# Kernel tuning notes

Measured on AMD Instinct MI355X. Metric: run time of the kernel, lower is better.

Reference implementation:

```python
import jax, jax.numpy as jnp
import numpy as np

EMBED_DIM = 1024
NUM_HEADS = 16
HEAD_DIM = EMBED_DIM // NUM_HEADS
TGT_LEN = 1024
SRC_LEN = 1024
BSZ = 4


def setup_inputs() -> dict:
    key = jax.random.key(0)
    ks = jax.random.split(key, 7)
    query = jax.random.normal(ks[0], (TGT_LEN, BSZ, EMBED_DIM), dtype=jnp.float32)
    key_t = jax.random.normal(ks[1], (SRC_LEN, BSZ, EMBED_DIM), dtype=jnp.float32)
    # hard 0/1 multiplicative mask applied post-softmax
    hard_attention = jax.random.randint(ks[2], (BSZ, TGT_LEN, SRC_LEN), 0, 2).astype(jnp.float32)
    # xavier_uniform_ on [3E, E]
    limit = float(np.sqrt(6.0 / (3 * EMBED_DIM + EMBED_DIM)))
    in_proj_weight = jax.random.uniform(ks[3], (3 * EMBED_DIM, EMBED_DIM), dtype=jnp.float32,
                                        minval=-limit, maxval=limit)
    in_proj_bias = jnp.zeros((3 * EMBED_DIM,), dtype=jnp.float32)
    limit_o = float(np.sqrt(1.0 / EMBED_DIM))
    out_proj_weight = jax.random.uniform(ks[4], (EMBED_DIM, EMBED_DIM), dtype=jnp.float32,
                                         minval=-limit_o, maxval=limit_o)
    out_proj_bias = jnp.zeros((EMBED_DIM,), dtype=jnp.float32)
    return {
        "query": query,
        "key": key_t,
        "hard_attention": hard_attention,
        "in_proj_weight": in_proj_weight,
        "in_proj_bias": in_proj_bias,
        "out_proj_weight": out_proj_weight,
        "out_proj_bias": out_proj_bias,
    }


def reference(query, key, hard_attention, in_proj_weight, in_proj_bias,
              out_proj_weight, out_proj_bias):
    tgt_len, bsz, embed_dim = query.shape
    src_len = key.shape[0]
    h, hd = NUM_HEADS, embed_dim // NUM_HEADS
    scaling = float(hd) ** -0.5

    # QKV projections (F.linear uses y = x @ W.T + b)
    wq = in_proj_weight[:embed_dim]
    wkv = in_proj_weight[embed_dim:]
    bq = in_proj_bias[:embed_dim]
    bkv = in_proj_bias[embed_dim:]
    q = jnp.einsum('tbe,fe->tbf', query, wq) + bq          # [T,B,E]
    kv = jnp.einsum('sbe,fe->sbf', key, wkv) + bkv          # [S,B,2E]
    k, v = jnp.split(kv, 2, axis=-1)

    q = (q * scaling).reshape(tgt_len, bsz, h, hd).transpose(1, 2, 0, 3)  # [B,H,T,D]
    k = k.reshape(src_len, bsz, h, hd).transpose(1, 2, 0, 3)              # [B,H,S,D]
    v = v.reshape(src_len, bsz, h, hd).transpose(1, 2, 0, 3)              # [B,H,S,D]

    scores = jnp.einsum('bhtd,bhsd->bhts', q, k)            # [B,H,T,S]
    attn = jax.nn.softmax(scores, axis=-1)
    # dropout_p = 0.0 -> identity
    attn = attn * hard_attention[:, None, :, :]             # post-softmax hard mask

    out = jnp.einsum('bhts,bhsd->bhtd', attn, v)            # [B,H,T,D]
    out = out.transpose(2, 0, 1, 3).reshape(tgt_len, bsz, embed_dim)
    out = jnp.einsum('tbe,fe->tbf', out, out_proj_weight) + out_proj_bias

    avg_weights = attn.sum(axis=1) / h                      # [B,T,S]
    return (out, avg_weights)
```

## Files before the change

kernel.cpp:

```cpp
#include <hip/hip_runtime.h>
#include <cstdint>
#include <cstddef>

typedef __bf16 bf16x8 __attribute__((ext_vector_type(8)));
typedef float  f32x4  __attribute__((ext_vector_type(4)));
typedef unsigned short u16x8 __attribute__((ext_vector_type(8)));

__device__ __forceinline__ uint16_t f2bf(float f) {
  uint32_t u = __float_as_uint(f);
  u += 0x7fffu + ((u >> 16) & 1u);
  return (uint16_t)(u >> 16);
}
__device__ __forceinline__ float bf2f(uint16_t u) {
  return __uint_as_float((uint32_t)u << 16);
}
__device__ __forceinline__ uint32_t cvtpk(float lo, float hi) {
  uint32_t r;
  asm("v_cvt_pk_bf16_f32 %0, %1, %2" : "=v"(r) : "v"(lo), "v"(hi));
  return r;
}

__device__ __forceinline__ f32x4 mfma16(bf16x8 a, bf16x8 b, f32x4 c) {
  return __builtin_amdgcn_mfma_f32_16x16x32_bf16(a, b, c, 0, 0, 0);
}

#define GLD_TO_LDS16(gptr, lptr)                                                   \
  __builtin_amdgcn_global_load_lds(                                                \
      (const __attribute__((address_space(1))) void*)(gptr),                       \
      (__attribute__((address_space(3))) void*)(lptr), 16, 0, 0)

__global__ void prep(const float* __restrict__ q, const float* __restrict__ k,
                     const float* __restrict__ w, const float* __restrict__ wo,
                     const float* __restrict__ hard,
                     uint16_t* __restrict__ Xq, uint16_t* __restrict__ Xk,
                     uint16_t* __restrict__ Wb, uint16_t* __restrict__ Wob,
                     uint32_t* __restrict__ bits) {
  const int bid = blockIdx.x;
  if (bid < 12288) {
    int i = bid * 256 + threadIdx.x;
    const float* src;
    uint16_t* dst;
    int off;
    if (i < 1048576)      { src = q;  dst = Xq;  off = i; }
    else if (i < 2097152) { src = k;  dst = Xk;  off = i - 1048576; }
    else if (i < 2883584) { src = w;  dst = Wb;  off = i - 2097152; }
    else                  { src = wo; dst = Wob; off = i - 2883584; }
    float4 v = ((const float4*)src)[off];
    ushort4 o;
    o.x = f2bf(v.x); o.y = f2bf(v.y); o.z = f2bf(v.z); o.w = f2bf(v.w);
    ((ushort4*)dst)[off] = o;
  } else {
    int base = (bid - 12288) * 1024;
#pragma unroll
    for (int c = 0; c < 4; c++) {
      int i = base + c * 256 + threadIdx.x;
      unsigned long long m = __ballot(hard[i] != 0.0f);
      if ((threadIdx.x & 63) == 0) {
        int wd = i >> 5;
        bits[wd]     = (uint32_t)m;
        bits[wd + 1] = (uint32_t)(m >> 32);
      }
    }
  }
}

__global__ __launch_bounds__(256)
void gemm_qkv(const uint16_t* __restrict__ Xq, const uint16_t* __restrict__ Xk,
              const uint16_t* __restrict__ Wb, const float* __restrict__ ipb,
              uint16_t* __restrict__ Qb, uint16_t* __restrict__ Kb,
              uint16_t* __restrict__ Vt) {
  __shared__ __align__(16) char As[128 * 128];
  __shared__ __align__(16) char Bs[128 * 128];
  const int tid  = threadIdx.x;
  const int wave = tid >> 6, lane = tid & 63;
  const int quad = lane >> 4, l16 = lane & 15;
  const int sw = (l16 & 7) << 4;

  const int swz = (blockIdx.x & 7) * 96 + (blockIdx.x >> 3);
  const uint16_t *A, *B;
  const float* bias;
  int bm, bn, mode;
  if (swz < 256) {
    mode = 0; A = Xq; B = Wb; bias = ipb;
    bm = swz >> 3; bn = swz & 7;
  } else {
    mode = 1; A = Xk; B = Wb + (1 << 20); bias = ipb + 1024;
    int t = swz - 256; bm = t >> 4; bn = t & 15;
  }
  const int wm = (wave >> 1) << 6, wn = (wave & 1) << 6;

  const int lrow = lane >> 3;
  const int scol = ((lane & 7) ^ lrow) << 4;
  const char* Ag = (const char*)A + (size_t)(bm * 128) * 2048;
  const char* Bg = (const char*)B + (size_t)(bn * 128) * 2048;

  f32x4 acc[4][4] = {};

  for (int k0 = 0; k0 < 2048; k0 += 128) {
    __syncthreads();
#pragma unroll
    for (int j = 0; j < 4; j++) {
      const int rbase = j * 32 + wave * 8;
      GLD_TO_LDS16(Ag + (size_t)(rbase + lrow) * 2048 + k0 + scol,
                   As + rbase * 128);
      GLD_TO_LDS16(Bg + (size_t)(rbase + lrow) * 2048 + k0 + scol,
                   Bs + rbase * 128);
    }
    __syncthreads();

    bf16x8 af[4][2], bfr[4][2];
#pragma unroll
    for (int i = 0; i < 4; i++) {
      const char* pa = As + (wm + i * 16 + l16) * 128;
      const char* pb = Bs + (wn + i * 16 + l16) * 128;
#pragma unroll
      for (int ks = 0; ks < 2; ks++) {
        af[i][ks]  = *(const bf16x8*)(pa + ((ks * 64 + quad * 16) ^ sw));
        bfr[i][ks] = *(const bf16x8*)(pb + ((ks * 64 + quad * 16) ^ sw));
      }
    }
#pragma unroll
    for (int ks = 0; ks < 2; ks++)
#pragma unroll
      for (int mi = 0; mi < 4; mi++)
#pragma unroll
        for (int ni = 0; ni < 4; ni++)
          acc[mi][ni] = mfma16(af[mi][ks], bfr[ni][ks], acc[mi][ni]);
  }

#pragma unroll
  for (int mi = 0; mi < 4; mi++)
#pragma unroll
    for (int ni = 0; ni < 4; ni++)
#pragma unroll
      for (int r = 0; r < 4; r++) {
        int gi = bm * 128 + wm + mi * 16 + quad * 4 + r;
        int gf = bn * 128 + wn + ni * 16 + l16;
        float c = acc[mi][ni][r] + bias[gf];
        if (mode == 0) {
          c *= 0.125f;
          int t = gi >> 2, b = gi & 3, h = gf >> 6, d = gf & 63;
          Qb[((((size_t)b * 16 + h) * 1024 + t) << 6) + d] = f2bf(c);
        } else {
          int s = gi >> 2, b = gi & 3;
          if (gf < 1024) {
            int h = gf >> 6, d = gf & 63;
            Kb[((((size_t)b * 16 + h) * 1024 + s) << 6) + d] = f2bf(c);
          } else {
            int fv = gf - 1024, h = fv >> 6, d = fv & 63;
            Vt[((((size_t)b * 16 + h) * 64 + d) << 10) + s] = f2bf(c);
          }
        }
      }
}

__global__ __launch_bounds__(256, 2)
void attn_kernel(const uint16_t* __restrict__ qb, const uint16_t* __restrict__ kb,
                 const uint16_t* __restrict__ vtb, const uint32_t* __restrict__ bits,
                 uint16_t* __restrict__ attn_out, float* __restrict__ rlout) {
  __shared__ __align__(16) uint16_t Ks[128 * 64];
  __shared__ __align__(16) uint16_t Vs[64 * 128];
  __shared__ __align__(16) uint16_t Pb[4 * 32 * 128];

  const int bid = blockIdx.x;
  const int xcd = bid & 7, j = bid >> 3;
  const int slab = xcd * 8 + (j >> 3);
  const int b = slab >> 4, h = slab & 15;
  const int t0 = (j & 7) << 7;
  const int tid = threadIdx.x, wave = tid >> 6, lane = tid & 63;
  const int quad = lane >> 4, l16 = lane & 15;
  const int sw = (l16 & 7) << 4;
  const size_t bh = (size_t)b * 16 + h;
  const int tw = t0 + wave * 32;
  const int ta = tw + l16, tb = ta + 16;
  char* PwA = (char*)(Pb + wave * (32 * 128)) + l16 * 256;
  char* PwB = PwA + 16 * 256;

  const uint16_t* qA = qb + ((bh << 10) + ta) * 64;
  bf16x8 aqA0 = *(const bf16x8*)(qA + quad * 8);
  bf16x8 aqA1 = *(const bf16x8*)(qA + 32 + quad * 8);
  bf16x8 aqB0 = *(const bf16x8*)(qA + 1024 + quad * 8);
  bf16x8 aqB1 = *(const bf16x8*)(qA + 1024 + 32 + quad * 8);

  f32x4 accA[4] = {}, accB[4] = {};
  float smA = 0.f, smB = 0.f;

  const int kr = tid >> 3, kc8 = tid & 7;
  const int vr = tid >> 4, vc16 = tid & 15;

  const uint32_t* bA = bits + (((size_t)(b << 10) + ta) << 5);
  const uint32_t* bB = bits + (((size_t)(b << 10) + tb) << 5);

  u16x8 kreg[4], vreg[4];
#pragma unroll
  for (int r = 0; r < 4; r++)
    kreg[r] = *(const u16x8*)(kb + (bh << 16) + (size_t)(r * 256 + tid) * 8);
#pragma unroll
  for (int r = 0; r < 4; r++)
    vreg[r] = *(const u16x8*)(vtb + (((bh << 6) + r * 16 + vr) << 10) + vc16 * 8);
  uint4 uA = *(const uint4*)bA;
  uint4 uB = *(const uint4*)bB;

  for (int sc = 0; sc < 8; sc++) {
    uint32_t wA[4] = {uA.x >> (quad * 4), uA.y >> (quad * 4),
                      uA.z >> (quad * 4), uA.w >> (quad * 4)};
    uint32_t wB[4] = {uB.x >> (quad * 4), uB.y >> (quad * 4),
                      uB.z >> (quad * 4), uB.w >> (quad * 4)};

    __syncthreads();
#pragma unroll
    for (int r = 0; r < 4; r++) {
      const int row = r * 32 + kr;
      *(u16x8*)((char*)Ks + row * 128 + ((kc8 * 16) ^ ((row & 7) << 4))) = kreg[r];
    }
#pragma unroll
    for (int r = 0; r < 4; r++) {
      const int row = r * 16 + vr;
      *(u16x8*)((char*)Vs + row * 256 + ((vc16 * 16) ^ ((row & 7) << 4))) = vreg[r];
    }
    __syncthreads();

    if (sc < 7) {
      const uint16_t* kbase = kb + (bh << 16) + (size_t)(sc + 1) * 8192;
#pragma unroll
      for (int r = 0; r < 4; r++)
        kreg[r] = *(const u16x8*)(kbase + (size_t)(r * 256 + tid) * 8);
#pragma unroll
      for (int r = 0; r < 4; r++)
        vreg[r] = *(const u16x8*)(vtb + (((bh << 6) + r * 16 + vr) << 10) +
                                  (sc + 1) * 128 + vc16 * 8);
      uA = *(const uint4*)(bA + (sc + 1) * 4);
      uB = *(const uint4*)(bB + (sc + 1) * 4);
    }

#pragma unroll
    for (int nn = 0; nn < 8; nn++) {
      const char* kbp = (const char*)Ks + (nn * 16 + l16) * 128;
      bf16x8 bk0 = *(const bf16x8*)(kbp + ((quad * 16) ^ sw));
      bf16x8 bk1 = *(const bf16x8*)(kbp + ((64 + quad * 16) ^ sw));
      f32x4 cA = {}, cB = {};
      cA = mfma16(bk0, aqA0, cA); cA = mfma16(bk1, aqA1, cA);
      cB = mfma16(bk0, aqB0, cB); cB = mfma16(bk1, aqB1, cB);
      const uint32_t mA = wA[nn >> 1] >> ((nn & 1) * 16);
      const uint32_t mB = wB[nn >> 1] >> ((nn & 1) * 16);
      float eA[4], eB[4];
#pragma unroll
      for (int r = 0; r < 4; r++) {
        eA[r] = __expf(cA[r]); smA += eA[r];
        eB[r] = __expf(cB[r]); smB += eB[r];
        eA[r] = ((mA >> r) & 1) ? eA[r] : 0.f;
        eB[r] = ((mB >> r) & 1) ? eB[r] : 0.f;
      }
      const int pc = (nn * 32 + quad * 8) ^ sw;
      *(uint2*)(PwA + pc) = make_uint2(cvtpk(eA[0], eA[1]), cvtpk(eA[2], eA[3]));
      *(uint2*)(PwB + pc) = make_uint2(cvtpk(eB[0], eB[1]), cvtpk(eB[2], eB[3]));
    }

#pragma unroll
    for (int kc = 0; kc < 4; kc++) {
      const int pcb = (kc * 64 + quad * 16) ^ sw;
      bf16x8 apA = *(const bf16x8*)(PwA + pcb);
      bf16x8 apB = *(const bf16x8*)(PwB + pcb);
#pragma unroll
      for (int dt = 0; dt < 4; dt++) {
        bf16x8 bv = *(const bf16x8*)((const char*)Vs + (dt * 16 + l16) * 256 +
                                     ((kc * 64 + quad * 16) ^ sw));
        accA[dt] = mfma16(bv, apA, accA[dt]);
        accB[dt] = mfma16(bv, apB, accB[dt]);
      }
    }
  }

  smA += __shfl_xor(smA, 16); smA += __shfl_xor(smA, 32);
  smB += __shfl_xor(smB, 16); smB += __shfl_xor(smB, 32);
  const float rlA = 1.0f / smA, rlB = 1.0f / smB;
  if (quad == 0) rlout[(bh << 10) + ta] = rlA;
  if (quad == 1) rlout[(bh << 10) + tb] = rlB;

#pragma unroll
  for (int dt = 0; dt < 4; dt++) {
    uint2 oA = make_uint2(cvtpk(accA[dt][0] * rlA, accA[dt][1] * rlA),
                          cvtpk(accA[dt][2] * rlA, accA[dt][3] * rlA));
    *(uint2*)(attn_out + ((size_t)(ta * 4 + b) << 10) + h * 64 + dt * 16 + quad * 4) = oA;
    uint2 oB = make_uint2(cvtpk(accB[dt][0] * rlB, accB[dt][1] * rlB),
                          cvtpk(accB[dt][2] * rlB, accB[dt][3] * rlB));
    *(uint2*)(attn_out + ((size_t)(tb * 4 + b) << 10) + h * 64 + dt * 16 + quad * 4) = oB;
  }
}

__global__ __launch_bounds__(256, 4)
void tail(const uint16_t* __restrict__ qb, const uint16_t* __restrict__ kb,
          const float* __restrict__ rlin, const float* __restrict__ hard,
          const uint16_t* __restrict__ Ao, const uint16_t* __restrict__ Bw,
          const float* __restrict__ opb,
          float* __restrict__ out, float* __restrict__ avgout) {
  __shared__ __align__(16) char smem[16384];
  const int bid = blockIdx.x;
  const int tid = threadIdx.x, wave = tid >> 6, lane = tid & 63;
  const int quad = lane >> 4, l16 = lane & 15;

  if (bid < 512) {
    uint16_t* Ks = (uint16_t*)smem;
    const int xcd = bid & 7, j = bid >> 3;
    const int b  = xcd >> 1;
    const int t0 = ((xcd & 1) * 8 + (j >> 3)) << 6;
    const int s0 = (j & 7) << 7;
    const int sw = (l16 & 7) << 4;
    const int tr = t0 + wave * 16 + l16;
    const int kr = tid >> 3, kc8 = tid & 7;

    float av[8][4] = {};

    u16x8 kreg[4];
    {
      const uint16_t* kb0 = kb + ((((size_t)b * 16) << 10) + s0) * 64;
#pragma unroll
      for (int r = 0; r < 4; r++)
        kreg[r] = *(const u16x8*)(kb0 + (size_t)(r * 256 + tid) * 8);
    }

    for (int hh = 0; hh < 16; hh++) {
      __syncthreads();
#pragma unroll
      for (int r = 0; r < 4; r++) {
        const int row = r * 32 + kr;
        *(u16x8*)((char*)Ks + row * 128 + ((kc8 * 16) ^ ((row & 7) << 4))) = kreg[r];
      }
      __syncthreads();
      if (hh < 15) {
        const uint16_t* kb2 = kb + ((((size_t)b * 16 + hh + 1) << 10) + s0) * 64;
#pragma unroll
        for (int r = 0; r < 4; r++)
          kreg[r] = *(const u16x8*)(kb2 + (size_t)(r * 256 + tid) * 8);
      }

      const size_t bh = (size_t)b * 16 + hh;
      const uint16_t* qrow = qb + ((bh << 10) + tr) * 64;
      bf16x8 aq0 = *(const bf16x8*)(qrow + quad * 8);
      bf16x8 aq1 = *(const bf16x8*)(qrow + 32 + quad * 8);
      const float rl = rlin[(bh << 10) + tr];

#pragma unroll
      for (int n = 0; n < 8; n++) {
        const char* kbp = (const char*)Ks + (n * 16 + l16) * 128;
        bf16x8 bk0 = *(const bf16x8*)(kbp + ((quad * 16) ^ sw));
        bf16x8 bk1 = *(const bf16x8*)(kbp + ((64 + quad * 16) ^ sw));
        f32x4 c = {};
        c = mfma16(bk0, aq0, c);
        c = mfma16(bk1, aq1, c);
#pragma unroll
        for (int r = 0; r < 4; r++) av[n][r] += __expf(c[r]) * rl;
      }
    }

    const float* hrow = hard + (((size_t)(b << 10) + tr) << 10) + s0 + quad * 4;
    float* orow = avgout + ((size_t)(b << 10) + tr) * 1024 + s0 + quad * 4;
#pragma unroll
    for (int n = 0; n < 8; n++) {
      float4 hm = *(const float4*)(hrow + n * 16);
      float4 f;
      f.x = av[n][0] * (hm.x != 0.f ? 0.0625f : 0.f);
      f.y = av[n][1] * (hm.y != 0.f ? 0.0625f : 0.f);
      f.z = av[n][2] * (hm.z != 0.f ? 0.0625f : 0.f);
      f.w = av[n][3] * (hm.w != 0.f ? 0.0625f : 0.f);
      *(float4*)(orow + n * 16) = f;
    }
  } else {
    uint16_t* As = (uint16_t*)smem;
    uint16_t* Bs = (uint16_t*)(smem + 4096);
    const int u = bid - 512;
    const int swz = (u & 7) * 64 + (u >> 3);
    const int bm = swz >> 3, bn = swz & 7;
    const int wm = (wave >> 1) << 5, wn = (wave & 1) << 6;
    const int K = 1024;

    f32x4 acc[2][4] = {};

    for (int k0 = 0; k0 < K; k0 += 32) {
      __syncthreads();
      {
        int c   = wave * 64 + lane;
        int row = c >> 2, kc = c & 3;
        const uint16_t* ga = Ao + (size_t)(bm * 64 + row) * K + k0 + kc * 8;
        GLD_TO_LDS16(ga, As + (size_t)(wave * 64) * 8);
      }
#pragma unroll
      for (int jj = 0; jj < 2; jj++) {
        int c   = wave * 128 + jj * 64 + lane;
        int row = c >> 2, kc = c & 3;
        const uint16_t* gb = Bw + (size_t)(bn * 128 + row) * K + k0 + kc * 8;
        GLD_TO_LDS16(gb, Bs + (size_t)(wave * 128 + jj * 64) * 8);
      }
      __syncthreads();

      bf16x8 af[2], bfr[4];
#pragma unroll
      for (int i = 0; i < 2; i++)
        af[i] = *(const bf16x8*)(As + (wm + i * 16 + l16) * 32 + quad * 8);
#pragma unroll
      for (int i = 0; i < 4; i++)
        bfr[i] = *(const bf16x8*)(Bs + (wn + i * 16 + l16) * 32 + quad * 8);
#pragma unroll
      for (int mi = 0; mi < 2; mi++)
#pragma unroll
        for (int ni = 0; ni < 4; ni++)
          acc[mi][ni] = mfma16(af[mi], bfr[ni], acc[mi][ni]);
    }

#pragma unroll
    for (int mi = 0; mi < 2; mi++)
#pragma unroll
      for (int ni = 0; ni < 4; ni++)
#pragma unroll
        for (int r = 0; r < 4; r++) {
          int gi = bm * 64 + wm + mi * 16 + quad * 4 + r;
          int gf = bn * 128 + wn + ni * 16 + l16;
          out[(size_t)gi * 1024 + gf] = acc[mi][ni][r] + opb[gf];
        }
  }
}

extern "C" void kernel_launch(void* const* d_in, const int* in_sizes, int n_in,
                              void* d_out, int out_size, void* d_ws, size_t ws_size,
                              hipStream_t stream) {
  const float* query = (const float*)d_in[0];
  const float* key   = (const float*)d_in[1];
  const float* hard  = (const float*)d_in[2];
  const float* ipw   = (const float*)d_in[3];
  const float* ipb   = (const float*)d_in[4];
  const float* opw   = (const float*)d_in[5];
  const float* opb   = (const float*)d_in[6];

  char* ws = (char*)d_ws;
  const size_t MB = 1ull << 20;
  uint16_t* Xq  = (uint16_t*)(ws + 0);
  uint16_t* Xk  = (uint16_t*)(ws + 8 * MB);
  uint16_t* Wb  = (uint16_t*)(ws + 16 * MB);
  uint16_t* Wob = (uint16_t*)(ws + 22 * MB);
  uint16_t* Qb  = (uint16_t*)(ws + 24 * MB);
  uint16_t* Kb  = (uint16_t*)(ws + 32 * MB);
  uint16_t* Vt  = (uint16_t*)(ws + 40 * MB);
  uint16_t* AO  = Xq;
  float*    rlws = (float*)(ws + 8 * MB);

  float* out = (float*)d_out;
  float* avg = out + 4194304;
  uint32_t* bits = (uint32_t*)out;

  prep<<<16384, 256, 0, stream>>>(query, key, ipw, opw, hard,
                                  Xq, Xk, Wb, Wob, bits);

  gemm_qkv<<<768, 256, 0, stream>>>(Xq, Xk, Wb, ipb, Qb, Kb, Vt);

  attn_kernel<<<512, 256, 0, stream>>>(Qb, Kb, Vt, bits, AO, rlws);

  tail<<<1024, 256, 0, stream>>>(Qb, Kb, rlws, hard, AO, Wob, opb, out, avg);
}
```

Measured before the change: 227.6 us.

## Deepen out-projection GEMM K-tile with XOR-swizzled LDS and remap avg-weight blocks

The output-projection GEMM branch of the tail kernel now stages 64 bf16 K-elements per iteration instead of 32, using an XOR swizzle on the LDS column to avoid bank conflicts. It issues two MFMA k-steps per barrier pair, which halves the number of syncs and global-to-LDS rounds. Shared memory grows to 24 KB. The avg-weights branch also remaps block indices so each XCD handles contiguous (batch, source-slab) groups, aiming for better L2 locality of K data. The larger LDS footprint may reduce occupancy.

```diff
diff --git a/kernel.cpp b/kernel.cpp
--- a/kernel.cpp
+++ b/kernel.cpp
@@ -294,7 +294,7 @@
           const uint16_t* __restrict__ Ao, const uint16_t* __restrict__ Bw,
           const float* __restrict__ opb,
           float* __restrict__ out, float* __restrict__ avgout) {
-  __shared__ __align__(16) char smem[16384];
+  __shared__ __align__(16) char smem[24576];
   const int bid = blockIdx.x;
   const int tid = threadIdx.x, wave = tid >> 6, lane = tid & 63;
   const int quad = lane >> 4, l16 = lane & 15;
@@ -302,9 +302,10 @@
   if (bid < 512) {
     uint16_t* Ks = (uint16_t*)smem;
     const int xcd = bid & 7, j = bid >> 3;
-    const int b  = xcd >> 1;
-    const int t0 = ((xcd & 1) * 8 + (j >> 3)) << 6;
-    const int s0 = (j & 7) << 7;
+    const int slab = xcd * 4 + (j >> 4);
+    const int b  = slab >> 3;
+    const int s0 = (slab & 7) << 7;
+    const int t0 = (j & 15) << 6;
     const int sw = (l16 & 7) << 4;
     const int tr = t0 + wave * 16 + l16;
     const int kr = tid >> 3, kc8 = tid & 7;
@@ -366,45 +367,58 @@
       *(float4*)(orow + n * 16) = f;
     }
   } else {
-    uint16_t* As = (uint16_t*)smem;
-    uint16_t* Bs = (uint16_t*)(smem + 4096);
+    char* As = smem;
+    char* Bs = smem + 8192;
     const int u = bid - 512;
     const int swz = (u & 7) * 64 + (u >> 3);
     const int bm = swz >> 3, bn = swz & 7;
     const int wm = (wave >> 1) << 5, wn = (wave & 1) << 6;
-    const int K = 1024;
+    const int sw = (l16 & 7) << 4;
+    const int lrow = lane >> 3;
+    const int scol = ((lane & 7) ^ lrow) << 4;
+    const char* Ag = (const char*)Ao + (size_t)(bm * 64) * 2048;
+    const char* Bg = (const char*)Bw + (size_t)(bn * 128) * 2048;
 
     f32x4 acc[2][4] = {};
 
-    for (int k0 = 0; k0 < K; k0 += 32) {
+    for (int k0 = 0; k0 < 2048; k0 += 128) {
       __syncthreads();
-      {
-        int c   = wave * 64 + lane;
-        int row = c >> 2, kc = c & 3;
-        const uint16_t* ga = Ao + (size_t)(bm * 64 + row) * K + k0 + kc * 8;
-        GLD_TO_LDS16(ga, As + (size_t)(wave * 64) * 8);
-      }
 #pragma unroll
       for (int jj = 0; jj < 2; jj++) {
-        int c   = wave * 128 + jj * 64 + lane;
-        int row = c >> 2, kc = c & 3;
-        const uint16_t* gb = Bw + (size_t)(bn * 128 + row) * K + k0 + kc * 8;
-        GLD_TO_LDS16(gb, Bs + (size_t)(wave * 128 + jj * 64) * 8);
+        const int rbase = jj * 32 + wave * 8;
+        GLD_TO_LDS16(Ag + (size_t)(rbase + lrow) * 2048 + k0 + scol,
+                     As + rbase * 128);
+      }
+#pragma unroll
+      for (int jj = 0; jj < 4; jj++) {
+        const int rbase = jj * 32 + wave * 8;
+        GLD_TO_LDS16(Bg + (size_t)(rbase + lrow) * 2048 + k0 + scol,
+                     Bs + rbase * 128);
       }
       __syncthreads();
 
-      bf16x8 af[2], bfr[4];
-#pragma unroll
-      for (int i = 0; i < 2; i++)
-        af[i] = *(const bf16x8*)(As + (wm + i * 16 + l16) * 32 + quad * 8);
-#pragma unroll
-      for (int i = 0; i < 4; i++)
-        bfr[i] = *(const bf16x8*)(Bs + (wn + i * 16 + l16) * 32 + quad * 8);
-#pragma unroll
-      for (int mi = 0; mi < 2; mi++)
-#pragma unroll
-        for (int ni = 0; ni < 4; ni++)
-          acc[mi][ni] = mfma16(af[mi], bfr[ni], acc[mi][ni]);
+      bf16x8 af[2][2], bfr[4][2];
+#pragma unroll
+      for (int i = 0; i < 2; i++) {
+        const char* pa = As + (wm + i * 16 + l16) * 128;
+#pragma unroll
+        for (int ks = 0; ks < 2; ks++)
+          af[i][ks] = *(const bf16x8*)(pa + ((ks * 64 + quad * 16) ^ sw));
+      }
+#pragma unroll
+      for (int i = 0; i < 4; i++) {
+        const char* pb = Bs + (wn + i * 16 + l16) * 128;
+#pragma unroll
+        for (int ks = 0; ks < 2; ks++)
+          bfr[i][ks] = *(const bf16x8*)(pb + ((ks * 64 + quad * 16) ^ sw));
+      }
+#pragma unroll
+      for (int ks = 0; ks < 2; ks++)
+#pragma unroll
+        for (int mi = 0; mi < 2; mi++)
+#pragma unroll
+          for (int ni = 0; ni < 4; ni++)
+            acc[mi][ni] = mfma16(af[mi][ks], bfr[ni][ks], acc[mi][ni]);
     }
 
 #pragma unroll
```

Measured after the change: 228.8 us. Within noise of the previous version (+0.5%).
